# Kernel optimization log

Measured on AMD Instinct MI355X. Metric: run time of the kernel, lower is better.

Reference implementation:

```python
import jax, jax.numpy as jnp
import numpy as np
from jax import lax

CHUNK = 64          # rows per chunk in the parabola pass (bounds peak memory)
INF = jnp.float32(1e12)  # 'no site in this column' sentinel for squared distance


def _edt_sq(mask):
    """Exact squared Euclidean distance transform of a 2D bool mask.

    Matches scipy.ndimage.distance_transform_edt(mask)**2: for pixels where
    mask is True (nonzero), squared distance to the nearest False (zero)
    pixel; 0 at False pixels. Separable: 1D along-column distance, then a
    brute-force lower-envelope (parabola) pass along rows, which is exact.
    """
    h, w = mask.shape
    sites = ~mask  # zero pixels = distance sources
    idx = jnp.arange(h, dtype=jnp.int32)[:, None]  # [H,1]
    # distance (in rows) to nearest site above / below in the same column
    up = idx - lax.cummax(jnp.where(sites, idx, -h), axis=0)
    down = lax.cummin(jnp.where(sites, idx, 2 * h), axis=0, reverse=True) - idx
    d = jnp.minimum(up, down)  # >= h means no site in this column
    g = jnp.where(d >= h, INF, d.astype(jnp.float32) ** 2)  # [H,W]

    # parabola pass along axis 1: out[r, j] = min_k g[r, k] + (j-k)^2
    j = jnp.arange(w, dtype=jnp.float32)
    dk2 = (j[:, None] - j[None, :]) ** 2  # [W_j, W_k]

    def row_chunk(gc):  # gc: [CHUNK, W]
        return jnp.min(gc[:, None, :] + dk2[None, :, :], axis=-1)

    gch = g.reshape(h // CHUNK, CHUNK, w)
    return lax.map(row_chunk, gch).reshape(h, w)


def _signed_distance(t):
    """t: bool foreground mask. Returns inside*(~t) - (outside-1)*t, where
    outside = EDT(t) (fg pixel -> nearest bg) and inside = EDT(~t)
    (bg pixel -> nearest fg), as in the original distance_metric."""
    outside = jnp.sqrt(_edt_sq(t))
    inside = jnp.sqrt(_edt_sq(~t))
    tf = t.astype(jnp.float32)
    return inside * (1.0 - tf) - (outside - 1.0) * tf


def setup_inputs() -> dict:
    key = jax.random.key(0)
    k1, k2 = jax.random.split(key)
    inp = jax.random.normal(k1, (1024, 1024), dtype=jnp.float32)
    target = jax.random.randint(k2, (1024, 1024), 0, 2, dtype=jnp.int32)
    return {"input": inp, "target": target}


def reference(input, target):
    sd = _signed_distance(target != 0)
    return jnp.mean(input * sd)
```

## Files before the change

### kernel.cpp

```cpp
#include <hip/hip_runtime.h>

#define H 1024
#define W 1024
#define NPIX (H * W)
#define WW 16
#define INF_F 1e12f
#define THREADS 256
#define BIG (1 << 29)

__device__ __noinline__ int vert_dist_full(const unsigned long long* __restrict__ pw,
                                           int r, int c, int pol) {
  int w = r >> 6, b = r & 63;
  unsigned long long v = pw[w * W + c];
  unsigned long long m_c = pol ? v : ~v;
  int dup = 1 << 30, ddn = 1 << 30;
  unsigned long long am = m_c & ((1ULL << b) - 1ULL);
  if (am) {
    dup = b - (63 - __builtin_clzll(am));
  } else {
    for (int ww = w - 1; ww >= 0; --ww) {
      unsigned long long mv = pw[ww * W + c];
      mv = pol ? mv : ~mv;
      if (mv) { dup = r - (ww * 64 + 63 - __builtin_clzll(mv)); break; }
    }
  }
  unsigned long long bm = m_c >> b;
  if (bm) {
    ddn = __builtin_ctzll(bm);
  } else {
    for (int ww = w + 1; ww < WW; ++ww) {
      unsigned long long mv = pw[ww * W + c];
      mv = pol ? mv : ~mv;
      if (mv) { ddn = (ww * 64 + __builtin_ctzll(mv)) - r; break; }
    }
  }
  return min(dup, ddn);
}

__device__ __noinline__ int horiz_exact(const unsigned long long* __restrict__ pw,
                                        int r, int c, int pol, int best, int dk0) {
  for (int dk = dk0; dk < W; ++dk) {
    int dk2 = dk * dk;
    if (dk2 >= best) break;
    if (c - dk >= 0) {
      int d = vert_dist_full(pw, r, c - dk, pol);
      if (d < H) best = min(best, d * d + dk2);
    }
    if (c + dk < W) {
      int d = vert_dist_full(pw, r, c + dk, pol);
      if (d < H) best = min(best, d * d + dk2);
    }
  }
  return best;
}

__global__ __launch_bounds__(THREADS) void pack_bits(
    const int* __restrict__ target, unsigned int* __restrict__ pw32) {
  int tg = blockIdx.x * THREADS + threadIdx.x;
  int w = tg >> 11;
  int half = (tg >> 10) & 1;
  int c = tg & (W - 1);
  int rbase = w * 64 + half * 32;
  unsigned int val = 0;
#pragma unroll
  for (int b = 0; b < 32; ++b) {
    if (target[(rbase + b) * W + c] != 0) val |= (1u << b);
  }
  pw32[((w * W + c) << 1) + half] = val;
}

__global__ __launch_bounds__(THREADS) void fused_edt(
    const unsigned long long* __restrict__ pw,
    const float* __restrict__ input,
    double* __restrict__ partials) {
  __shared__ unsigned char sd8[8][W + 64];
  const int tid = threadIdx.x;
  const int r0 = blockIdx.x << 2;
  const int w = r0 >> 6, b0 = r0 & 63;
  const int c0 = tid << 2;

  if (tid < 128) {
    int p = tid >> 4, q = tid & 15;
    ((unsigned int*)sd8)[p * 272 + (q < 8 ? q : 256 + q)] = 0xFFFFFFFFu;
  }

  unsigned long long curv[4], prevv[4], nextv[4];
  *(ulonglong2*)&curv[0] = *(const ulonglong2*)(pw + w * W + c0);
  *(ulonglong2*)&curv[2] = *(const ulonglong2*)(pw + w * W + c0 + 2);
  const bool hp = (w > 0), hn = (w < WW - 1);
  if (hp) {
    *(ulonglong2*)&prevv[0] = *(const ulonglong2*)(pw + (w - 1) * W + c0);
    *(ulonglong2*)&prevv[2] = *(const ulonglong2*)(pw + (w - 1) * W + c0 + 2);
  } else prevv[0] = prevv[1] = prevv[2] = prevv[3] = 0ULL;
  if (hn) {
    *(ulonglong2*)&nextv[0] = *(const ulonglong2*)(pw + (w + 1) * W + c0);
    *(ulonglong2*)&nextv[2] = *(const ulonglong2*)(pw + (w + 1) * W + c0 + 2);
  } else nextv[0] = nextv[1] = nextv[2] = nextv[3] = 0ULL;

  unsigned char dloc[2][4][4];
#pragma unroll
  for (int pol = 0; pol < 2; ++pol) {
#pragma unroll
    for (int k = 0; k < 4; ++k) {
      unsigned long long m_c = pol ? curv[k] : ~curv[k];
      unsigned long long m_p = hp ? (pol ? prevv[k] : ~prevv[k]) : 0ULL;
      unsigned long long m_n = hn ? (pol ? nextv[k] : ~nextv[k]) : 0ULL;
#pragma unroll
      for (int rr = 0; rr < 4; ++rr) {
        int b = b0 + rr;
        int d = 1 << 30;
        unsigned long long am = m_c & ((1ULL << b) - 1ULL);
        if (am) d = b - (63 - __builtin_clzll(am));
        else if (m_p) d = b + 1 + __builtin_clzll(m_p);
        unsigned long long bm = m_c >> b;
        int dd = 1 << 30;
        if (bm) dd = __builtin_ctzll(bm);
        else if (m_n) dd = (64 - b) + __builtin_ctzll(m_n);
        d = min(d, dd);
        if (d > 64) d = vert_dist_full(pw, r0 + rr, c0 + k, pol);
        dloc[pol][rr][k] = (unsigned char)min(d, 255);
      }
    }
  }
#pragma unroll
  for (int pol = 0; pol < 2; ++pol)
#pragma unroll
    for (int rr = 0; rr < 4; ++rr) {
      unsigned int u = (unsigned int)dloc[pol][rr][0] |
                       ((unsigned int)dloc[pol][rr][1] << 8) |
                       ((unsigned int)dloc[pol][rr][2] << 16) |
                       ((unsigned int)dloc[pol][rr][3] << 24);
      *(unsigned int*)&sd8[pol * 4 + rr][32 + c0] = u;
    }
  __syncthreads();

  double val = 0.0;
#pragma unroll
  for (int rr = 0; rr < 4; ++rr) {
    const float4 iv = *(const float4*)(input + (r0 + rr) * W + c0);
    const float ivk[4] = {iv.x, iv.y, iv.z, iv.w};
#pragma unroll
    for (int k = 0; k < 4; ++k) {
      const bool t = (dloc[1][rr][k] == 0);
      const int pol = t ? 0 : 1;
      const int own = t ? dloc[0][rr][k] : dloc[1][rr][k];
      int best = (own == 255) ? BIG : own * own;
      const unsigned char* __restrict__ sg = &sd8[pol * 4 + rr][32 + c0 + k];
      for (int dk = 1; dk <= 32; ++dk) {
        int dk2 = dk * dk;
        if (dk2 >= best) break;
        int dl = sg[-dk], dr = sg[dk];
        int gl = (dl == 255) ? BIG : dl * dl;
        int gr = (dr == 255) ? BIG : dr * dr;
        best = min(best, min(gl, gr) + dk2);
      }
      if (best > 1089) {
        int r = r0 + rr, c = c0 + k;
        if (best > 65025) {
          int ov = vert_dist_full(pw, r, c, pol);
          best = (ov < H) ? ov * ov : (1 << 30);
          best = horiz_exact(pw, r, c, pol, best, 1);
        } else {
          best = horiz_exact(pw, r, c, pol, best, 33);
        }
      }
      float bestf = (best >= BIG) ? INF_F : (float)best;
      float dist = sqrtf(bestf);
      float sd = t ? (1.0f - dist) : dist;
      val += (double)(ivk[k] * sd);
    }
  }

  for (int off = 32; off > 0; off >>= 1)
    val += __shfl_down(val, off, 64);
  __shared__ double smem[THREADS / 64];
  int lane = tid & 63, wid = tid >> 6;
  if (lane == 0) smem[wid] = val;
  __syncthreads();
  if (tid == 0)
    partials[blockIdx.x] = smem[0] + smem[1] + smem[2] + smem[3];
}

__global__ __launch_bounds__(THREADS) void reduce_partials(
    const double* __restrict__ partials, float* __restrict__ out) {
  double s = partials[threadIdx.x];
  for (int off = 32; off > 0; off >>= 1)
    s += __shfl_down(s, off, 64);
  __shared__ double smem[THREADS / 64];
  int lane = threadIdx.x & 63, wid = threadIdx.x >> 6;
  if (lane == 0) smem[wid] = s;
  __syncthreads();
  if (threadIdx.x == 0)
    out[0] = (float)((smem[0] + smem[1] + smem[2] + smem[3]) / (double)NPIX);
}

extern "C" void kernel_launch(void* const* d_in, const int* in_sizes, int n_in,
                              void* d_out, int out_size, void* d_ws, size_t ws_size,
                              hipStream_t stream) {
  const float* input = (const float*)d_in[0];
  const int* target = (const int*)d_in[1];
  float* out = (float*)d_out;

  double* partials = (double*)d_ws;
  unsigned long long* pw = (unsigned long long*)((char*)d_ws + 4096);

  pack_bits<<<128, THREADS, 0, stream>>>(target, (unsigned int*)pw);
  fused_edt<<<H / 4, THREADS, 0, stream>>>(pw, input, partials);
  reduce_partials<<<1, THREADS, 0, stream>>>(partials, out);
}
```

Baseline: 69.59 us.

## Process one row per block to launch four times more blocks

The fused EDT kernel now handles a single row per block instead of four, so the grid grows from 256 to 1024 blocks and there are more waves to spread across CUs. Per-thread register arrays and shared memory shrink to match. The first two horizontal offsets are unrolled without the early-exit check, and the final reduction sums four partials per thread. The trade is that the prev/cur/next bit words are reloaded for every row, and the per-block setup and barrier now repeat for every row.

```diff
diff --git a/kernel.cpp b/kernel.cpp
--- a/kernel.cpp
+++ b/kernel.cpp
@@ -69,17 +69,17 @@
   pw32[((w * W + c) << 1) + half] = val;
 }
 
-__global__ __launch_bounds__(THREADS) void fused_edt(
+__global__ __launch_bounds__(THREADS) void fused_edt_row(
     const unsigned long long* __restrict__ pw,
     const float* __restrict__ input,
     double* __restrict__ partials) {
-  __shared__ unsigned char sd8[8][W + 64];
+  __shared__ unsigned char sd8[2][W + 64];
   const int tid = threadIdx.x;
-  const int r0 = blockIdx.x << 2;
-  const int w = r0 >> 6, b0 = r0 & 63;
+  const int r = blockIdx.x;
+  const int w = r >> 6, b = r & 63;
   const int c0 = tid << 2;
 
-  if (tid < 128) {
+  if (tid < 32) {
     int p = tid >> 4, q = tid & 15;
     ((unsigned int*)sd8)[p * 272 + (q < 8 ? q : 256 + q)] = 0xFFFFFFFFu;
   }
@@ -97,7 +97,7 @@
     *(ulonglong2*)&nextv[2] = *(const ulonglong2*)(pw + (w + 1) * W + c0 + 2);
   } else nextv[0] = nextv[1] = nextv[2] = nextv[3] = 0ULL;
 
-  unsigned char dloc[2][4][4];
+  unsigned char dloc[2][4];
 #pragma unroll
   for (int pol = 0; pol < 2; ++pol) {
 #pragma unroll
@@ -105,70 +105,68 @@
       unsigned long long m_c = pol ? curv[k] : ~curv[k];
       unsigned long long m_p = hp ? (pol ? prevv[k] : ~prevv[k]) : 0ULL;
       unsigned long long m_n = hn ? (pol ? nextv[k] : ~nextv[k]) : 0ULL;
-#pragma unroll
-      for (int rr = 0; rr < 4; ++rr) {
-        int b = b0 + rr;
-        int d = 1 << 30;
-        unsigned long long am = m_c & ((1ULL << b) - 1ULL);
-        if (am) d = b - (63 - __builtin_clzll(am));
-        else if (m_p) d = b + 1 + __builtin_clzll(m_p);
-        unsigned long long bm = m_c >> b;
-        int dd = 1 << 30;
-        if (bm) dd = __builtin_ctzll(bm);
-        else if (m_n) dd = (64 - b) + __builtin_ctzll(m_n);
-        d = min(d, dd);
-        if (d > 64) d = vert_dist_full(pw, r0 + rr, c0 + k, pol);
-        dloc[pol][rr][k] = (unsigned char)min(d, 255);
+      int d = 1 << 30;
+      unsigned long long am = m_c & ((1ULL << b) - 1ULL);
+      if (am) d = b - (63 - __builtin_clzll(am));
+      else if (m_p) d = b + 1 + __builtin_clzll(m_p);
+      unsigned long long bm = m_c >> b;
+      int dd = 1 << 30;
+      if (bm) dd = __builtin_ctzll(bm);
+      else if (m_n) dd = (64 - b) + __builtin_ctzll(m_n);
+      d = min(d, dd);
+      if (d > 64) d = vert_dist_full(pw, r, c0 + k, pol);
+      dloc[pol][k] = (unsigned char)min(d, 255);
+    }
+  }
+#pragma unroll
+  for (int pol = 0; pol < 2; ++pol) {
+    unsigned int u = (unsigned int)dloc[pol][0] |
+                     ((unsigned int)dloc[pol][1] << 8) |
+                     ((unsigned int)dloc[pol][2] << 16) |
+                     ((unsigned int)dloc[pol][3] << 24);
+    *(unsigned int*)&sd8[pol][32 + c0] = u;
+  }
+  __syncthreads();
+
+  double val = 0.0;
+  const float4 iv = *(const float4*)(input + r * W + c0);
+  const float ivk[4] = {iv.x, iv.y, iv.z, iv.w};
+#pragma unroll
+  for (int k = 0; k < 4; ++k) {
+    const bool t = (dloc[1][k] == 0);
+    const int pol = t ? 0 : 1;
+    const int own = dloc[pol][k];
+    int best = (own == 255) ? BIG : own * own;
+    const unsigned char* __restrict__ sg = &sd8[pol][32 + c0 + k];
+#pragma unroll
+    for (int dk = 1; dk <= 2; ++dk) {
+      int dl = sg[-dk], dr = sg[dk];
+      int gl = (dl == 255) ? BIG : dl * dl;
+      int gr = (dr == 255) ? BIG : dr * dr;
+      best = min(best, min(gl, gr) + dk * dk);
+    }
+    for (int dk = 3; dk <= 32; ++dk) {
+      int dk2 = dk * dk;
+      if (dk2 >= best) break;
+      int dl = sg[-dk], dr = sg[dk];
+      int gl = (dl == 255) ? BIG : dl * dl;
+      int gr = (dr == 255) ? BIG : dr * dr;
+      best = min(best, min(gl, gr) + dk2);
+    }
+    if (best > 1089) {
+      int c = c0 + k;
+      if (best > 65025) {
+        int ov = vert_dist_full(pw, r, c, pol);
+        best = (ov < H) ? ov * ov : (1 << 30);
+        best = horiz_exact(pw, r, c, pol, best, 1);
+      } else {
+        best = horiz_exact(pw, r, c, pol, best, 33);
       }
     }
-  }
-#pragma unroll
-  for (int pol = 0; pol < 2; ++pol)
-#pragma unroll
-    for (int rr = 0; rr < 4; ++rr) {
-      unsigned int u = (unsigned int)dloc[pol][rr][0] |
-                       ((unsigned int)dloc[pol][rr][1] << 8) |
-                       ((unsigned int)dloc[pol][rr][2] << 16) |
-                       ((unsigned int)dloc[pol][rr][3] << 24);
-      *(unsigned int*)&sd8[pol * 4 + rr][32 + c0] = u;
-    }
-  __syncthreads();
-
-  double val = 0.0;
-#pragma unroll
-  for (int rr = 0; rr < 4; ++rr) {
-    const float4 iv = *(const float4*)(input + (r0 + rr) * W + c0);
-    const float ivk[4] = {iv.x, iv.y, iv.z, iv.w};
-#pragma unroll
-    for (int k = 0; k < 4; ++k) {
-      const bool t = (dloc[1][rr][k] == 0);
-      const int pol = t ? 0 : 1;
-      const int own = t ? dloc[0][rr][k] : dloc[1][rr][k];
-      int best = (own == 255) ? BIG : own * own;
-      const unsigned char* __restrict__ sg = &sd8[pol * 4 + rr][32 + c0 + k];
-      for (int dk = 1; dk <= 32; ++dk) {
-        int dk2 = dk * dk;
-        if (dk2 >= best) break;
-        int dl = sg[-dk], dr = sg[dk];
-        int gl = (dl == 255) ? BIG : dl * dl;
-        int gr = (dr == 255) ? BIG : dr * dr;
-        best = min(best, min(gl, gr) + dk2);
-      }
-      if (best > 1089) {
-        int r = r0 + rr, c = c0 + k;
-        if (best > 65025) {
-          int ov = vert_dist_full(pw, r, c, pol);
-          best = (ov < H) ? ov * ov : (1 << 30);
-          best = horiz_exact(pw, r, c, pol, best, 1);
-        } else {
-          best = horiz_exact(pw, r, c, pol, best, 33);
-        }
-      }
-      float bestf = (best >= BIG) ? INF_F : (float)best;
-      float dist = sqrtf(bestf);
-      float sd = t ? (1.0f - dist) : dist;
-      val += (double)(ivk[k] * sd);
-    }
+    float bestf = (best >= BIG) ? INF_F : (float)best;
+    float dist = sqrtf(bestf);
+    float sd = t ? (1.0f - dist) : dist;
+    val += (double)(ivk[k] * sd);
   }
 
   for (int off = 32; off > 0; off >>= 1)
@@ -183,7 +181,9 @@
 
 __global__ __launch_bounds__(THREADS) void reduce_partials(
     const double* __restrict__ partials, float* __restrict__ out) {
-  double s = partials[threadIdx.x];
+  double s = 0.0;
+#pragma unroll
+  for (int i = 0; i < 4; ++i) s += partials[threadIdx.x + i * THREADS];
   for (int off = 32; off > 0; off >>= 1)
     s += __shfl_down(s, off, 64);
   __shared__ double smem[THREADS / 64];
@@ -202,9 +202,9 @@
   float* out = (float*)d_out;
 
   double* partials = (double*)d_ws;
-  unsigned long long* pw = (unsigned long long*)((char*)d_ws + 4096);
+  unsigned long long* pw = (unsigned long long*)((char*)d_ws + 8192);
 
   pack_bits<<<128, THREADS, 0, stream>>>(target, (unsigned int*)pw);
-  fused_edt<<<H / 4, THREADS, 0, stream>>>(pw, input, partials);
+  fused_edt_row<<<H, THREADS, 0, stream>>>(pw, input, partials);
   reduce_partials<<<1, THREADS, 0, stream>>>(partials, out);
 }
```

New measurement: 66.60 us. -4.3%, faster.
